# Optimization experiments

Hardware: AMD Instinct MI355X
Metric: run time of the kernel (lower is better)

Reference implementation:

```python
import jax, jax.numpy as jnp
import numpy as np

H = 64          # HIDDEN_SIZE
D = 300         # WORD_VEC_DIMS
L = 3           # NUM_LSTM_LAYERS
B = 256
T = 512


def _uniform(key, shape, scale):
    return jax.random.uniform(key, shape, jnp.float32, -scale, scale)


def setup_inputs() -> dict:
    key = jax.random.key(0)
    keys = jax.random.split(key, 32)
    s = 1.0 / np.sqrt(H)  # torch LSTM/Linear init scale
    inp = {
        "input": jax.random.normal(keys[0], (B, T, D), jnp.float32),
        "h_0": jnp.zeros((L, B, H), jnp.float32),
        "c_0": jnp.zeros((L, B, H), jnp.float32),
    }
    k = 1
    for l in range(L):
        din = D if l == 0 else H
        inp[f"wih{l}"] = _uniform(keys[k], (4 * H, din), s); k += 1
        inp[f"whh{l}"] = _uniform(keys[k], (4 * H, H), s); k += 1
        inp[f"bih{l}"] = _uniform(keys[k], (4 * H,), s); k += 1
        inp[f"bhh{l}"] = _uniform(keys[k], (4 * H,), s); k += 1
    inp["w1"] = _uniform(keys[k], (H, H), s); k += 1
    inp["b1"] = _uniform(keys[k], (H,), s); k += 1
    inp["w2"] = _uniform(keys[k], (D, H), s); k += 1
    inp["b2"] = _uniform(keys[k], (D,), s); k += 1
    return inp


def _lstm_layer(x_tbd, h0, c0, Wih, Whh, bih, bhh):
    # x_tbd: [T, B, Din]; precompute input projection outside the scan
    xp = jnp.einsum('tbd,gd->tbg', x_tbd, Wih) + bih  # [T, B, 4H]

    def step(carry, xt):
        h, c = carry
        g = xt + h @ Whh.T + bhh
        i, f, gg, o = jnp.split(g, 4, axis=-1)  # torch gate order: i,f,g,o
        c = jax.nn.sigmoid(f) * c + jax.nn.sigmoid(i) * jnp.tanh(gg)
        h = jax.nn.sigmoid(o) * jnp.tanh(c)
        return (h, c), h

    (hT, cT), hs = jax.lax.scan(step, (h0, c0), xp)
    return hs, hT, cT  # hs: [T, B, H]


def reference(input, h_0, c_0, wih0, whh0, bih0, bhh0, wih1, whh1, bih1, bhh1,
              wih2, whh2, bih2, bhh2, w1, b1, w2, b2):
    wih = [wih0, wih1, wih2]
    whh = [whh0, whh1, whh2]
    bih = [bih0, bih1, bih2]
    bhh = [bhh0, bhh1, bhh2]
    x = jnp.transpose(input, (1, 0, 2))  # [T, B, D]
    hs_n, cs_n = [], []
    for l in range(L):
        x, hT, cT = _lstm_layer(x, h_0[l], c_0[l], wih[l], whh[l], bih[l], bhh[l])
        hs_n.append(hT)
        cs_n.append(cT)
    # x is now [T, B, H] == output.permute(1, 0, 2) of the batch_first LSTM.
    # Faithfully replicate the original permute+view reordering:
    flat = x.reshape(-1, H)                       # time-major flatten
    y = jnp.tanh(flat @ w1.T + b1) @ w2.T + b2    # MLP head
    out = y.reshape(input.shape[0], -1, D)        # reinterpreted batch-major
    h_n = jnp.stack(hs_n)
    c_n = jnp.stack(cs_n)
    return out, h_n, c_n
```

## Files before the change

### kernel.cpp

```cpp
#include <hip/hip_runtime.h>
#include <math.h>


#define TT 512
#define BB 256
#define DD 300
#define HH 64
#define MM (TT * BB)
#define XP 256
#define TC 128
#define NC (TT / TC)

__device__ __forceinline__ float bf2f(unsigned short u) {
    return __uint_as_float(((unsigned int)u) << 16);
}
__device__ __forceinline__ unsigned short f2bf(float f) {
    unsigned int x = __float_as_uint(f);
    x += 0x7FFFu + ((x >> 16) & 1u);
    return (unsigned short)(x >> 16);
}
__device__ __forceinline__ float sigm(float x) { return 1.f / (1.f + __expf(-x)); }
__device__ __forceinline__ float tanh_f(float x) { return 1.f - 2.f / (__expf(2.f * x) + 1.f); }

__device__ __forceinline__ float ld1(const void* p, long long i, int md) {
    return md ? ((const float*)p)[i] : bf2f(((const unsigned short*)p)[i]);
}
__device__ __forceinline__ void ld4v(float* d, const void* p, long long i, int md) {
    if (md) {
        float4 v = *(const float4*)((const float*)p + i);
        d[0] = v.x; d[1] = v.y; d[2] = v.z; d[3] = v.w;
    } else {
        ushort4 u = *(const ushort4*)((const unsigned short*)p + i);
        d[0] = bf2f(u.x); d[1] = bf2f(u.y); d[2] = bf2f(u.z); d[3] = bf2f(u.w);
    }
}

#define FMA4x4(a, bv)                                        \
    acc[0][0] = fmaf((a).x, (bv).x, acc[0][0]);              \
    acc[0][1] = fmaf((a).x, (bv).y, acc[0][1]);              \
    acc[0][2] = fmaf((a).x, (bv).z, acc[0][2]);              \
    acc[0][3] = fmaf((a).x, (bv).w, acc[0][3]);              \
    acc[1][0] = fmaf((a).y, (bv).x, acc[1][0]);              \
    acc[1][1] = fmaf((a).y, (bv).y, acc[1][1]);              \
    acc[1][2] = fmaf((a).y, (bv).z, acc[1][2]);              \
    acc[1][3] = fmaf((a).y, (bv).w, acc[1][3]);              \
    acc[2][0] = fmaf((a).z, (bv).x, acc[2][0]);              \
    acc[2][1] = fmaf((a).z, (bv).y, acc[2][1]);              \
    acc[2][2] = fmaf((a).z, (bv).z, acc[2][2]);              \
    acc[2][3] = fmaf((a).z, (bv).w, acc[2][3]);              \
    acc[3][0] = fmaf((a).w, (bv).x, acc[3][0]);              \
    acc[3][1] = fmaf((a).w, (bv).y, acc[3][1]);              \
    acc[3][2] = fmaf((a).w, (bv).z, acc[3][2]);              \
    acc[3][3] = fmaf((a).w, (bv).w, acc[3][3]);

__global__ void detect_kernel(const void* inp, int* mode) {
    if (threadIdx.x == 0 && blockIdx.x == 0) {
        const unsigned short* u = (const unsigned short*)inp;
        int bad = 0;
        for (int i = 0; i < 256; ++i) {
            float f = bf2f(u[i]);
            if (!(f == f) || fabsf(f) > 1e6f) ++bad;
        }
        *mode = (bad >= 4) ? 1 : 0;
    }
}

__global__ __launch_bounds__(256) void init_state(
    const void* h0, const void* c0, float* hstate, float* cstate, const int* modep)
{
    const int md = *modep;
    int i = blockIdx.x * 256 + threadIdx.x;
    if (i < 3 * BB * HH) {
        hstate[i] = ld1(h0, i, md);
        cstate[i] = ld1(c0, i, md);
    }
}

__global__ __launch_bounds__(256) void final_state(
    const float* hstate, const float* cstate, void* out, const int* modep)
{
    const int md = *modep;
    int i = blockIdx.x * 256 + threadIdx.x;
    const long long base = (long long)MM * DD;
    if (i < 3 * BB * HH) {
        if (md) {
            ((float*)out)[base + i] = hstate[i];
            ((float*)out)[base + 3 * BB * HH + i] = cstate[i];
        } else {
            ((unsigned short*)out)[base + i] = f2bf(hstate[i]);
            ((unsigned short*)out)[base + 3 * BB * HH + i] = f2bf(cstate[i]);
        }
    }
}

__global__ __launch_bounds__(256) void proj0_chunk(
    const void* __restrict__ inp, const void* __restrict__ wih,
    const void* __restrict__ bih, const void* __restrict__ bhh,
    float* __restrict__ xp, const int* modep, int chunk)
{
    const int md = *modep;
    __shared__ __align__(16) float At[64][68];
    __shared__ __align__(16) float Wt[64][68];
    const int tid = threadIdx.x;
    const int lr = tid >> 2;
    const int lc = (tid & 3) * 16;
    const int tx = tid & 15, ty = tid >> 4;
    const int m0 = blockIdx.x * 64, n0 = blockIdx.y * 64;
    const int ml = m0 + lr;
    const int b = ml & 255;
    const int t = chunk * TC + (ml >> 8);
    const long long abase = (long long)b * (TT * DD) + (long long)t * DD;
    const long long wbase = (long long)(n0 + lr) * DD;
    float acc[4][4] = {{0.f,0.f,0.f,0.f},{0.f,0.f,0.f,0.f},{0.f,0.f,0.f,0.f},{0.f,0.f,0.f,0.f}};
    for (int k0 = 0; k0 < DD; k0 += 64) {
        if (k0 + lc + 15 < DD) {
            #pragma unroll
            for (int q = 0; q < 4; ++q) {
                float va[4], vw[4];
                ld4v(va, inp, abase + k0 + lc + q * 4, md);
                ld4v(vw, wih, wbase + k0 + lc + q * 4, md);
                #pragma unroll
                for (int e = 0; e < 4; ++e) {
                    At[lc + q * 4 + e][lr] = va[e];
                    Wt[lc + q * 4 + e][lr] = vw[e];
                }
            }
        } else {
            #pragma unroll
            for (int q = 0; q < 16; ++q) {
                int k = k0 + lc + q;
                At[lc + q][lr] = (k < DD) ? ld1(inp, abase + k, md) : 0.f;
                Wt[lc + q][lr] = (k < DD) ? ld1(wih, wbase + k, md) : 0.f;
            }
        }
        __syncthreads();
        #pragma unroll 16
        for (int k = 0; k < 64; ++k) {
            float4 a = *(const float4*)&At[k][ty * 4];
            float4 bv = *(const float4*)&Wt[k][tx * 4];
            FMA4x4(a, bv)
        }
        __syncthreads();
    }
    float bias[4];
    #pragma unroll
    for (int j = 0; j < 4; ++j) {
        int n = n0 + tx * 4 + j;
        bias[j] = ld1(bih, n, md) + ld1(bhh, n, md);
    }
    #pragma unroll
    for (int i = 0; i < 4; ++i) {
        long long row = m0 + ty * 4 + i;
        float4 o = make_float4(acc[i][0] + bias[0], acc[i][1] + bias[1],
                               acc[i][2] + bias[2], acc[i][3] + bias[3]);
        *(float4*)(xp + row * XP + n0 + tx * 4) = o;
    }
}

__global__ __launch_bounds__(256) void projh_chunk(
    const float* __restrict__ A, const void* __restrict__ wih,
    const void* __restrict__ bih, const void* __restrict__ bhh,
    float* __restrict__ xp, const int* modep)
{
    const int md = *modep;
    __shared__ __align__(16) float At[64][68];
    __shared__ __align__(16) float Wt[64][68];
    const int tid = threadIdx.x;
    const int lr = tid >> 2;
    const int lc = (tid & 3) * 16;
    const int tx = tid & 15, ty = tid >> 4;
    const int m0 = blockIdx.x * 64, n0 = blockIdx.y * 64;
    float acc[4][4] = {{0.f,0.f,0.f,0.f},{0.f,0.f,0.f,0.f},{0.f,0.f,0.f,0.f},{0.f,0.f,0.f,0.f}};
    #pragma unroll
    for (int q = 0; q < 4; ++q) {
        float4 av = *(const float4*)(A + (long long)(m0 + lr) * HH + lc + q * 4);
        float vw[4];
        ld4v(vw, wih, (long long)(n0 + lr) * HH + lc + q * 4, md);
        At[lc+q*4+0][lr]=av.x; At[lc+q*4+1][lr]=av.y; At[lc+q*4+2][lr]=av.z; At[lc+q*4+3][lr]=av.w;
        Wt[lc+q*4+0][lr]=vw[0]; Wt[lc+q*4+1][lr]=vw[1]; Wt[lc+q*4+2][lr]=vw[2]; Wt[lc+q*4+3][lr]=vw[3];
    }
    __syncthreads();
    #pragma unroll 16
    for (int k = 0; k < 64; ++k) {
        float4 a = *(const float4*)&At[k][ty * 4];
        float4 bv = *(const float4*)&Wt[k][tx * 4];
        FMA4x4(a, bv)
    }
    float bias[4];
    #pragma unroll
    for (int j = 0; j < 4; ++j) {
        int n = n0 + tx * 4 + j;
        bias[j] = ld1(bih, n, md) + ld1(bhh, n, md);
    }
    #pragma unroll
    for (int i = 0; i < 4; ++i) {
        long long row = m0 + ty * 4 + i;
        float4 o = make_float4(acc[i][0] + bias[0], acc[i][1] + bias[1],
                               acc[i][2] + bias[2], acc[i][3] + bias[3]);
        *(float4*)(xp + row * XP + n0 + tx * 4) = o;
    }
}

__global__ __launch_bounds__(256) void scan_chunk(
    const float* __restrict__ xp, float* __restrict__ hs,
    const void* __restrict__ whh,
    float* __restrict__ hstate, float* __restrict__ cstate, const int* modep)
{
    const int md = *modep;
    const int b = blockIdx.x;
    const int j = threadIdx.x;
    const int g = ((j & 3) << 6) | (j >> 2);
    const int m = j & 63;
    __shared__ __align__(16) float h_s[64];
    __shared__ __align__(16) float g_s[2][256];
    float w[64];
    #pragma unroll
    for (int q = 0; q < 16; ++q) {
        float v[4];
        ld4v(v, whh, (long long)g * HH + q * 4, md);
        w[4*q+0]=v[0]; w[4*q+1]=v[1]; w[4*q+2]=v[2]; w[4*q+3]=v[3];
    }
    float c = cstate[b * HH + m];
    h_s[m] = hstate[b * HH + m];
    float hval = h_s[m];

    const int type = j & 3;
    const float aa = (type == 2) ? 2.f : 1.f;
    const float cc = 1.f - aa;

    const long long xbase = (long long)b * XP + g;
    const long long xstep = (long long)BB * XP;
    float xc[8], xn[8];
    #pragma unroll
    for (int p = 0; p < 8; ++p) xc[p] = xp[xbase + (long long)p * xstep];

    for (int tg = 0; tg < TC; tg += 8) {
        if (tg + 8 < TC) {
            #pragma unroll
            for (int p = 0; p < 8; ++p)
                xn[p] = xp[xbase + (long long)(tg + 8 + p) * xstep];
        }
        #pragma unroll
        for (int u = 0; u < 8; ++u) {
            const int t = tg + u;
            float a0 = xc[u], a1 = 0.f, a2 = 0.f, a3 = 0.f;
            const float4* h4 = (const float4*)h_s;
            #pragma unroll
            for (int q = 0; q < 16; ++q) {
                float4 hv = h4[q];
                a0 = fmaf(hv.x, w[4*q+0], a0);
                a1 = fmaf(hv.y, w[4*q+1], a1);
                a2 = fmaf(hv.z, w[4*q+2], a2);
                a3 = fmaf(hv.w, w[4*q+3], a3);
            }
            float gr = (a0 + a1) + (a2 + a3);
            float s = 1.f / (1.f + __expf(-aa * gr));
            g_s[t & 1][j] = fmaf(aa, s, cc);
            asm volatile("s_waitcnt lgkmcnt(0)\n\ts_barrier" ::: "memory");
            float4 gv = *(const float4*)&g_s[t & 1][4 * m];
            c = gv.y * c + gv.x * gv.z;
            hval = gv.w * tanh_f(c);
            h_s[m] = hval;
            if (j < 64) hs[((long long)t * BB + b) * HH + m] = hval;
        }
        #pragma unroll
        for (int p = 0; p < 8; ++p) xc[p] = xn[p];
    }
    if (j < 64) {
        hstate[b * HH + m] = hval;
        cstate[b * HH + m] = c;
    }
}

__global__ __launch_bounds__(256) void head_chunk(
    const float* __restrict__ hs, const void* __restrict__ w1,
    const void* __restrict__ b1, const void* __restrict__ w2,
    const void* __restrict__ b2, void* __restrict__ out,
    const int* modep, int chunk)
{
    const int md = *modep;
    __shared__ __align__(16) float Ht[64][68];
    __shared__ __align__(16) float Wt[64][68];
    __shared__ __align__(16) float Zt[64][68];
    const int tid = threadIdx.x;
    const int lr = tid >> 2;
    const int lc = (tid & 3) * 16;
    const int tx = tid & 15, ty = tid >> 4;
    const int m0 = blockIdx.x * 64;
    const long long gbase = (long long)chunk * TC * BB;
    #pragma unroll
    for (int q = 0; q < 4; ++q) {
        float4 av = *(const float4*)(hs + (long long)(m0 + lr) * HH + lc + q * 4);
        float vw[4];
        ld4v(vw, w1, (long long)lr * HH + lc + q * 4, md);
        Ht[lc+q*4+0][lr]=av.x; Ht[lc+q*4+1][lr]=av.y; Ht[lc+q*4+2][lr]=av.z; Ht[lc+q*4+3][lr]=av.w;
        Wt[lc+q*4+0][lr]=vw[0]; Wt[lc+q*4+1][lr]=vw[1]; Wt[lc+q*4+2][lr]=vw[2]; Wt[lc+q*4+3][lr]=vw[3];
    }
    __syncthreads();
    {
        float acc[4][4] = {{0.f,0.f,0.f,0.f},{0.f,0.f,0.f,0.f},{0.f,0.f,0.f,0.f},{0.f,0.f,0.f,0.f}};
        #pragma unroll 16
        for (int k = 0; k < 64; ++k) {
            float4 a = *(const float4*)&Ht[k][ty * 4];
            float4 bv = *(const float4*)&Wt[k][tx * 4];
            FMA4x4(a, bv)
        }
        #pragma unroll
        for (int jj = 0; jj < 4; ++jj) {
            float bb = ld1(b1, tx * 4 + jj, md);
            #pragma unroll
            for (int ii = 0; ii < 4; ++ii)
                Zt[tx * 4 + jj][ty * 4 + ii] = tanh_f(acc[ii][jj] + bb);
        }
    }
    __syncthreads();
    for (int dt = 0; dt < 5; ++dt) {
        const int d0 = dt * 64;
        if (d0 + lr < DD) {
            #pragma unroll
            for (int q = 0; q < 4; ++q) {
                float vw[4];
                ld4v(vw, w2, (long long)(d0 + lr) * HH + lc + q * 4, md);
                Wt[lc+q*4+0][lr]=vw[0]; Wt[lc+q*4+1][lr]=vw[1];
                Wt[lc+q*4+2][lr]=vw[2]; Wt[lc+q*4+3][lr]=vw[3];
            }
        }
        __syncthreads();
        float acc[4][4] = {{0.f,0.f,0.f,0.f},{0.f,0.f,0.f,0.f},{0.f,0.f,0.f,0.f},{0.f,0.f,0.f,0.f}};
        #pragma unroll 16
        for (int k = 0; k < 64; ++k) {
            float4 a = *(const float4*)&Zt[k][ty * 4];
            float4 bv = *(const float4*)&Wt[k][tx * 4];
            FMA4x4(a, bv)
        }
        const int d = d0 + tx * 4;
        if (d < DD) {
            float bb0 = ld1(b2, d + 0, md), bb1 = ld1(b2, d + 1, md);
            float bb2v = ld1(b2, d + 2, md), bb3 = ld1(b2, d + 3, md);
            #pragma unroll
            for (int ii = 0; ii < 4; ++ii) {
                long long row = gbase + m0 + ty * 4 + ii;
                float o0 = acc[ii][0] + bb0, o1 = acc[ii][1] + bb1;
                float o2 = acc[ii][2] + bb2v, o3 = acc[ii][3] + bb3;
                if (md) {
                    *(float4*)((float*)out + row * DD + d) = make_float4(o0, o1, o2, o3);
                } else {
                    ushort4 o;
                    o.x = f2bf(o0); o.y = f2bf(o1); o.z = f2bf(o2); o.w = f2bf(o3);
                    *(ushort4*)((unsigned short*)out + row * DD + d) = o;
                }
            }
        }
        __syncthreads();
    }
}

extern "C" void kernel_launch(void* const* d_in, const int* in_sizes, int n_in,
                              void* d_out, int out_size, void* d_ws, size_t ws_size,
                              hipStream_t stream)
{
    const void* inp  = d_in[0];
    const void* h0   = d_in[1];
    const void* c0   = d_in[2];
    const void* wih0 = d_in[3];
    const void* whh0 = d_in[4];
    const void* bih0 = d_in[5];
    const void* bhh0 = d_in[6];
    const void* wih1 = d_in[7];
    const void* whh1 = d_in[8];
    const void* bih1 = d_in[9];
    const void* bhh1 = d_in[10];
    const void* wih2 = d_in[11];
    const void* whh2 = d_in[12];
    const void* bih2 = d_in[13];
    const void* bhh2 = d_in[14];
    const void* w1   = d_in[15];
    const void* b1   = d_in[16];
    const void* w2   = d_in[17];
    const void* b2   = d_in[18];

    int* mode = (int*)d_ws;
    float* wsf = (float*)d_ws;
    float* hstate = wsf + 16;
    float* cstate = hstate + 3 * BB * HH;
    float* xp  = cstate + 3 * BB * HH;
    float* hs0 = xp + (size_t)TC * BB * XP;
    float* hs1 = hs0 + (size_t)TC * BB * HH;
    float* hs2 = hs1 + (size_t)TC * BB * HH;

    detect_kernel<<<1, 64, 0, stream>>>(inp, mode);
    init_state<<<192, 256, 0, stream>>>(h0, c0, hstate, cstate, mode);

    for (int c = 0; c < NC; ++c) {
        proj0_chunk<<<dim3(TC * BB / 64, 4), 256, 0, stream>>>(
            inp, wih0, bih0, bhh0, xp, mode, c);
        scan_chunk<<<BB, 256, 0, stream>>>(
            xp, hs0, whh0, hstate, cstate, mode);
        projh_chunk<<<dim3(TC * BB / 64, 4), 256, 0, stream>>>(
            hs0, wih1, bih1, bhh1, xp, mode);
        scan_chunk<<<BB, 256, 0, stream>>>(
            xp, hs1, whh1, hstate + BB * HH, cstate + BB * HH, mode);
        projh_chunk<<<dim3(TC * BB / 64, 4), 256, 0, stream>>>(
            hs1, wih2, bih2, bhh2, xp, mode);
        scan_chunk<<<BB, 256, 0, stream>>>(
            xp, hs2, whh2, hstate + 2 * BB * HH, cstate + 2 * BB * HH, mode);
        head_chunk<<<TC * BB / 64, 256, 0, stream>>>(
            hs2, w1, b1, w2, b2, d_out, mode, c);
    }
    final_state<<<192, 256, 0, stream>>>(hstate, cstate, d_out, mode);
}
```

Measured before the change: 1.974 ms.

## Use split-bf16 MFMA for projections and head, shuffle-based LSTM gate exchange

Replaces the FP32 FMA tiled GEMMs in the input projections and MLP head with bf16 MFMA 16x16x32 instructions. To keep FP32-level accuracy, each operand is split into three bf16 parts and six cross products are accumulated. The weights are pre-split once by a new split_w kernel into workspace. The scan kernel now exchanges gate values through wave shuffles instead of a shared gate buffer, with a double-buffered h, and the hs buffers are merged into one. The split adds six MFMAs per tile plus conversion overhead, and the scan changes alter its synchronisation pattern.

```diff
diff --git a/kernel.cpp b/kernel.cpp
--- a/kernel.cpp
+++ b/kernel.cpp
@@ -11,6 +11,9 @@
 #define TC 128
 #define NC (TT / TC)
 
+typedef __attribute__((ext_vector_type(8))) short bf16x8;
+typedef __attribute__((ext_vector_type(4))) float f32x4;
+
 __device__ __forceinline__ float bf2f(unsigned short u) {
     return __uint_as_float(((unsigned int)u) << 16);
 }
@@ -19,7 +22,6 @@
     x += 0x7FFFu + ((x >> 16) & 1u);
     return (unsigned short)(x >> 16);
 }
-__device__ __forceinline__ float sigm(float x) { return 1.f / (1.f + __expf(-x)); }
 __device__ __forceinline__ float tanh_f(float x) { return 1.f - 2.f / (__expf(2.f * x) + 1.f); }
 
 __device__ __forceinline__ float ld1(const void* p, long long i, int md) {
@@ -35,23 +37,36 @@
     }
 }
 
-#define FMA4x4(a, bv)                                        \
-    acc[0][0] = fmaf((a).x, (bv).x, acc[0][0]);              \
-    acc[0][1] = fmaf((a).x, (bv).y, acc[0][1]);              \
-    acc[0][2] = fmaf((a).x, (bv).z, acc[0][2]);              \
-    acc[0][3] = fmaf((a).x, (bv).w, acc[0][3]);              \
-    acc[1][0] = fmaf((a).y, (bv).x, acc[1][0]);              \
-    acc[1][1] = fmaf((a).y, (bv).y, acc[1][1]);              \
-    acc[1][2] = fmaf((a).y, (bv).z, acc[1][2]);              \
-    acc[1][3] = fmaf((a).y, (bv).w, acc[1][3]);              \
-    acc[2][0] = fmaf((a).z, (bv).x, acc[2][0]);              \
-    acc[2][1] = fmaf((a).z, (bv).y, acc[2][1]);              \
-    acc[2][2] = fmaf((a).z, (bv).z, acc[2][2]);              \
-    acc[2][3] = fmaf((a).z, (bv).w, acc[2][3]);              \
-    acc[3][0] = fmaf((a).w, (bv).x, acc[3][0]);              \
-    acc[3][1] = fmaf((a).w, (bv).y, acc[3][1]);              \
-    acc[3][2] = fmaf((a).w, (bv).z, acc[3][2]);              \
-    acc[3][3] = fmaf((a).w, (bv).w, acc[3][3]);
+__device__ __forceinline__ f32x4 mfma16(bf16x8 a, bf16x8 b, f32x4 c) {
+    return __builtin_amdgcn_mfma_f32_16x16x32_bf16(a, b, c, 0, 0, 0);
+}
+
+__device__ __forceinline__ f32x4 mfma6(bf16x8 a1, bf16x8 a2, bf16x8 a3,
+                                       bf16x8 b1, bf16x8 b2, bf16x8 b3, f32x4 t) {
+    t = mfma16(a2, b2, t);
+    t = mfma16(a1, b3, t);
+    t = mfma16(a3, b1, t);
+    t = mfma16(a1, b2, t);
+    t = mfma16(a2, b1, t);
+    t = mfma16(a1, b1, t);
+    return t;
+}
+
+__device__ __forceinline__ void split3x4(const float* v, ushort4& h1, ushort4& h2, ushort4& h3) {
+    unsigned short a[4], b[4], c[4];
+    #pragma unroll
+    for (int e = 0; e < 4; ++e) {
+        unsigned short x = f2bf(v[e]);
+        float r1 = v[e] - bf2f(x);
+        unsigned short y = f2bf(r1);
+        float r2 = r1 - bf2f(y);
+        unsigned short z = f2bf(r2);
+        a[e] = x; b[e] = y; c[e] = z;
+    }
+    h1 = make_ushort4(a[0], a[1], a[2], a[3]);
+    h2 = make_ushort4(b[0], b[1], b[2], b[3]);
+    h3 = make_ushort4(c[0], c[1], c[2], c[3]);
+}
 
 __global__ void detect_kernel(const void* inp, int* mode) {
     if (threadIdx.x == 0 && blockIdx.x == 0) {
@@ -93,111 +108,178 @@
     }
 }
 
-__global__ __launch_bounds__(256) void proj0_chunk(
-    const void* __restrict__ inp, const void* __restrict__ wih,
+__global__ __launch_bounds__(256) void split_w(
+    const void* __restrict__ src, unsigned short* __restrict__ dst,
+    int rsrc, int csrc, int rdst, int cdst, const int* modep)
+{
+    const int md = *modep;
+    int i = blockIdx.x * 256 + threadIdx.x;
+    int n = rdst * cdst;
+    if (i >= n) return;
+    int r = i / cdst, cc = i - r * cdst;
+    float v = (r < rsrc && cc < csrc) ? ld1(src, (long long)r * csrc + cc, md) : 0.f;
+    unsigned short a = f2bf(v);
+    float r1 = v - bf2f(a);
+    unsigned short b = f2bf(r1);
+    float r2 = r1 - bf2f(b);
+    unsigned short c = f2bf(r2);
+    dst[i] = a; dst[n + i] = b; dst[2 * n + i] = c;
+}
+
+__global__ __launch_bounds__(256, 2) void proj0_chunk(
+    const void* __restrict__ inp, const unsigned short* __restrict__ wsp,
     const void* __restrict__ bih, const void* __restrict__ bhh,
     float* __restrict__ xp, const int* modep, int chunk)
 {
     const int md = *modep;
-    __shared__ __align__(16) float At[64][68];
-    __shared__ __align__(16) float Wt[64][68];
+    __shared__ __align__(16) unsigned short aS[3][64 * 40];
+    __shared__ __align__(16) unsigned short wS[3][256 * 40];
     const int tid = threadIdx.x;
-    const int lr = tid >> 2;
-    const int lc = (tid & 3) * 16;
-    const int tx = tid & 15, ty = tid >> 4;
-    const int m0 = blockIdx.x * 64, n0 = blockIdx.y * 64;
-    const int ml = m0 + lr;
+    const int m0 = blockIdx.x * 64;
+    const int lane = tid & 63, wv = tid >> 6;
+    const int fr = lane & 15, fq = lane >> 4;
+    const int ar = tid >> 2, acs = (tid & 3) * 8;
+    const int ml = m0 + ar;
     const int b = ml & 255;
     const int t = chunk * TC + (ml >> 8);
     const long long abase = (long long)b * (TT * DD) + (long long)t * DD;
-    const long long wbase = (long long)(n0 + lr) * DD;
-    float acc[4][4] = {{0.f,0.f,0.f,0.f},{0.f,0.f,0.f,0.f},{0.f,0.f,0.f,0.f},{0.f,0.f,0.f,0.f}};
-    for (int k0 = 0; k0 < DD; k0 += 64) {
-        if (k0 + lc + 15 < DD) {
-            #pragma unroll
-            for (int q = 0; q < 4; ++q) {
-                float va[4], vw[4];
-                ld4v(va, inp, abase + k0 + lc + q * 4, md);
-                ld4v(vw, wih, wbase + k0 + lc + q * 4, md);
+    float bias[4];
+    #pragma unroll
+    for (int nf = 0; nf < 4; ++nf) {
+        int n = wv * 64 + nf * 16 + fr;
+        bias[nf] = ld1(bih, n, md) + ld1(bhh, n, md);
+    }
+    f32x4 acc[4][4] = {};
+    for (int p = 0; p < 10; ++p) {
+        const int k0 = p * 32;
+        #pragma unroll
+        for (int q = 0; q < 2; ++q) {
+            const int kg = k0 + acs + q * 4;
+            float v[4];
+            if (kg + 3 < DD) {
+                ld4v(v, inp, abase + kg, md);
+            } else {
                 #pragma unroll
-                for (int e = 0; e < 4; ++e) {
-                    At[lc + q * 4 + e][lr] = va[e];
-                    Wt[lc + q * 4 + e][lr] = vw[e];
-                }
-            }
-        } else {
-            #pragma unroll
-            for (int q = 0; q < 16; ++q) {
-                int k = k0 + lc + q;
-                At[lc + q][lr] = (k < DD) ? ld1(inp, abase + k, md) : 0.f;
-                Wt[lc + q][lr] = (k < DD) ? ld1(wih, wbase + k, md) : 0.f;
-            }
+                for (int e = 0; e < 4; ++e)
+                    v[e] = (kg + e < DD) ? ld1(inp, abase + kg + e, md) : 0.f;
+            }
+            ushort4 h1, h2, h3;
+            split3x4(v, h1, h2, h3);
+            *(ushort4*)(&aS[0][ar * 40 + acs + q * 4]) = h1;
+            *(ushort4*)(&aS[1][ar * 40 + acs + q * 4]) = h2;
+            *(ushort4*)(&aS[2][ar * 40 + acs + q * 4]) = h3;
+        }
+        #pragma unroll
+        for (int pl = 0; pl < 3; ++pl) {
+            const uint4* gw = (const uint4*)(wsp + (size_t)pl * 81920 + (size_t)tid * 320 + k0);
+            uint4* dw = (uint4*)(&wS[pl][tid * 40]);
+            #pragma unroll
+            for (int qq = 0; qq < 4; ++qq) dw[qq] = gw[qq];
         }
         __syncthreads();
-        #pragma unroll 16
-        for (int k = 0; k < 64; ++k) {
-            float4 a = *(const float4*)&At[k][ty * 4];
-            float4 bv = *(const float4*)&Wt[k][tx * 4];
-            FMA4x4(a, bv)
+        bf16x8 wf[4][3];
+        #pragma unroll
+        for (int nf = 0; nf < 4; ++nf) {
+            #pragma unroll
+            for (int pl = 0; pl < 3; ++pl)
+                wf[nf][pl] = *(const bf16x8*)(&wS[pl][(wv * 64 + nf * 16 + fr) * 40 + fq * 8]);
+        }
+        #pragma unroll
+        for (int mf = 0; mf < 4; ++mf) {
+            bf16x8 a1 = *(const bf16x8*)(&aS[0][(mf * 16 + fr) * 40 + fq * 8]);
+            bf16x8 a2 = *(const bf16x8*)(&aS[1][(mf * 16 + fr) * 40 + fq * 8]);
+            bf16x8 a3 = *(const bf16x8*)(&aS[2][(mf * 16 + fr) * 40 + fq * 8]);
+            #pragma unroll
+            for (int nf = 0; nf < 4; ++nf)
+                acc[mf][nf] = mfma6(a1, a2, a3, wf[nf][0], wf[nf][1], wf[nf][2], acc[mf][nf]);
         }
         __syncthreads();
     }
-    float bias[4];
-    #pragma unroll
-    for (int j = 0; j < 4; ++j) {
-        int n = n0 + tx * 4 + j;
-        bias[j] = ld1(bih, n, md) + ld1(bhh, n, md);
-    }
-    #pragma unroll
-    for (int i = 0; i < 4; ++i) {
-        long long row = m0 + ty * 4 + i;
-        float4 o = make_float4(acc[i][0] + bias[0], acc[i][1] + bias[1],
-                               acc[i][2] + bias[2], acc[i][3] + bias[3]);
-        *(float4*)(xp + row * XP + n0 + tx * 4) = o;
-    }
-}
-
-__global__ __launch_bounds__(256) void projh_chunk(
-    const float* __restrict__ A, const void* __restrict__ wih,
+    #pragma unroll
+    for (int mf = 0; mf < 4; ++mf) {
+        #pragma unroll
+        for (int nf = 0; nf < 4; ++nf) {
+            const int col = wv * 64 + nf * 16 + fr;
+            #pragma unroll
+            for (int r = 0; r < 4; ++r) {
+                const int row = m0 + mf * 16 + fq * 4 + r;
+                xp[(long long)row * XP + col] = acc[mf][nf][r] + bias[nf];
+            }
+        }
+    }
+}
+
+__global__ __launch_bounds__(256, 2) void projh_chunk(
+    const float* __restrict__ A, const unsigned short* __restrict__ wsp,
     const void* __restrict__ bih, const void* __restrict__ bhh,
     float* __restrict__ xp, const int* modep)
 {
     const int md = *modep;
-    __shared__ __align__(16) float At[64][68];
-    __shared__ __align__(16) float Wt[64][68];
+    __shared__ __align__(16) unsigned short aS[3][64 * 40];
+    __shared__ __align__(16) unsigned short wS[3][256 * 40];
     const int tid = threadIdx.x;
-    const int lr = tid >> 2;
-    const int lc = (tid & 3) * 16;
-    const int tx = tid & 15, ty = tid >> 4;
-    const int m0 = blockIdx.x * 64, n0 = blockIdx.y * 64;
-    float acc[4][4] = {{0.f,0.f,0.f,0.f},{0.f,0.f,0.f,0.f},{0.f,0.f,0.f,0.f},{0.f,0.f,0.f,0.f}};
-    #pragma unroll
-    for (int q = 0; q < 4; ++q) {
-        float4 av = *(const float4*)(A + (long long)(m0 + lr) * HH + lc + q * 4);
-        float vw[4];
-        ld4v(vw, wih, (long long)(n0 + lr) * HH + lc + q * 4, md);
-        At[lc+q*4+0][lr]=av.x; At[lc+q*4+1][lr]=av.y; At[lc+q*4+2][lr]=av.z; At[lc+q*4+3][lr]=av.w;
-        Wt[lc+q*4+0][lr]=vw[0]; Wt[lc+q*4+1][lr]=vw[1]; Wt[lc+q*4+2][lr]=vw[2]; Wt[lc+q*4+3][lr]=vw[3];
-    }
-    __syncthreads();
-    #pragma unroll 16
-    for (int k = 0; k < 64; ++k) {
-        float4 a = *(const float4*)&At[k][ty * 4];
-        float4 bv = *(const float4*)&Wt[k][tx * 4];
-        FMA4x4(a, bv)
-    }
+    const int m0 = blockIdx.x * 64;
+    const int lane = tid & 63, wv = tid >> 6;
+    const int fr = lane & 15, fq = lane >> 4;
+    const int ar = tid >> 2, acs = (tid & 3) * 8;
     float bias[4];
     #pragma unroll
-    for (int j = 0; j < 4; ++j) {
-        int n = n0 + tx * 4 + j;
-        bias[j] = ld1(bih, n, md) + ld1(bhh, n, md);
-    }
-    #pragma unroll
-    for (int i = 0; i < 4; ++i) {
-        long long row = m0 + ty * 4 + i;
-        float4 o = make_float4(acc[i][0] + bias[0], acc[i][1] + bias[1],
-                               acc[i][2] + bias[2], acc[i][3] + bias[3]);
-        *(float4*)(xp + row * XP + n0 + tx * 4) = o;
+    for (int nf = 0; nf < 4; ++nf) {
+        int n = wv * 64 + nf * 16 + fr;
+        bias[nf] = ld1(bih, n, md) + ld1(bhh, n, md);
+    }
+    f32x4 acc[4][4] = {};
+    #pragma unroll
+    for (int p = 0; p < 2; ++p) {
+        const int k0 = p * 32;
+        #pragma unroll
+        for (int q = 0; q < 2; ++q) {
+            float v[4];
+            const float4 fv = *(const float4*)(A + (long long)(m0 + ar) * HH + k0 + acs + q * 4);
+            v[0] = fv.x; v[1] = fv.y; v[2] = fv.z; v[3] = fv.w;
+            ushort4 h1, h2, h3;
+            split3x4(v, h1, h2, h3);
+            *(ushort4*)(&aS[0][ar * 40 + acs + q * 4]) = h1;
+            *(ushort4*)(&aS[1][ar * 40 + acs + q * 4]) = h2;
+            *(ushort4*)(&aS[2][ar * 40 + acs + q * 4]) = h3;
+        }
+        #pragma unroll
+        for (int pl = 0; pl < 3; ++pl) {
+            const uint4* gw = (const uint4*)(wsp + (size_t)pl * 16384 + (size_t)tid * 64 + k0);
+            uint4* dw = (uint4*)(&wS[pl][tid * 40]);
+            #pragma unroll
+            for (int qq = 0; qq < 4; ++qq) dw[qq] = gw[qq];
+        }
+        __syncthreads();
+        bf16x8 wf[4][3];
+        #pragma unroll
+        for (int nf = 0; nf < 4; ++nf) {
+            #pragma unroll
+            for (int pl = 0; pl < 3; ++pl)
+                wf[nf][pl] = *(const bf16x8*)(&wS[pl][(wv * 64 + nf * 16 + fr) * 40 + fq * 8]);
+        }
+        #pragma unroll
+        for (int mf = 0; mf < 4; ++mf) {
+            bf16x8 a1 = *(const bf16x8*)(&aS[0][(mf * 16 + fr) * 40 + fq * 8]);
+            bf16x8 a2 = *(const bf16x8*)(&aS[1][(mf * 16 + fr) * 40 + fq * 8]);
+            bf16x8 a3 = *(const bf16x8*)(&aS[2][(mf * 16 + fr) * 40 + fq * 8]);
+            #pragma unroll
+            for (int nf = 0; nf < 4; ++nf)
+                acc[mf][nf] = mfma6(a1, a2, a3, wf[nf][0], wf[nf][1], wf[nf][2], acc[mf][nf]);
+        }
+        __syncthreads();
+    }
+    #pragma unroll
+    for (int mf = 0; mf < 4; ++mf) {
+        #pragma unroll
+        for (int nf = 0; nf < 4; ++nf) {
+            const int col = wv * 64 + nf * 16 + fr;
+            #pragma unroll
+            for (int r = 0; r < 4; ++r) {
+                const int row = m0 + mf * 16 + fq * 4 + r;
+                xp[(long long)row * XP + col] = acc[mf][nf][r] + bias[nf];
+            }
+        }
     }
 }
 
@@ -210,9 +292,10 @@
     const int b = blockIdx.x;
     const int j = threadIdx.x;
     const int g = ((j & 3) << 6) | (j >> 2);
+    const int i = j >> 2;
     const int m = j & 63;
-    __shared__ __align__(16) float h_s[64];
-    __shared__ __align__(16) float g_s[2][256];
+    const int bl = j & 60;
+    __shared__ __align__(16) float h_s[2][64];
     float w[64];
     #pragma unroll
     for (int q = 0; q < 16; ++q) {
@@ -220,9 +303,9 @@
         ld4v(v, whh, (long long)g * HH + q * 4, md);
         w[4*q+0]=v[0]; w[4*q+1]=v[1]; w[4*q+2]=v[2]; w[4*q+3]=v[3];
     }
-    float c = cstate[b * HH + m];
-    h_s[m] = hstate[b * HH + m];
-    float hval = h_s[m];
+    float c = cstate[b * HH + i];
+    h_s[0][m] = hstate[b * HH + m];
+    float hval = 0.f;
 
     const int type = j & 3;
     const float aa = (type == 2) ? 2.f : 1.f;
@@ -244,7 +327,7 @@
         for (int u = 0; u < 8; ++u) {
             const int t = tg + u;
             float a0 = xc[u], a1 = 0.f, a2 = 0.f, a3 = 0.f;
-            const float4* h4 = (const float4*)h_s;
+            const float4* h4 = (const float4*)h_s[t & 1];
             #pragma unroll
             for (int q = 0; q < 16; ++q) {
                 float4 hv = h4[q];
@@ -255,99 +338,135 @@
             }
             float gr = (a0 + a1) + (a2 + a3);
             float s = 1.f / (1.f + __expf(-aa * gr));
-            g_s[t & 1][j] = fmaf(aa, s, cc);
+            float y = fmaf(aa, s, cc);
+            float yi = __shfl(y, bl | 0);
+            float yf = __shfl(y, bl | 1);
+            float yg = __shfl(y, bl | 2);
+            float yo = __shfl(y, bl | 3);
+            c = yf * c + yi * yg;
+            hval = yo * tanh_f(c);
+            if ((j & 3) == 0) {
+                h_s[(t & 1) ^ 1][i] = hval;
+                hs[((long long)t * BB + b) * HH + i] = hval;
+            }
             asm volatile("s_waitcnt lgkmcnt(0)\n\ts_barrier" ::: "memory");
-            float4 gv = *(const float4*)&g_s[t & 1][4 * m];
-            c = gv.y * c + gv.x * gv.z;
-            hval = gv.w * tanh_f(c);
-            h_s[m] = hval;
-            if (j < 64) hs[((long long)t * BB + b) * HH + m] = hval;
         }
         #pragma unroll
         for (int p = 0; p < 8; ++p) xc[p] = xn[p];
     }
-    if (j < 64) {
-        hstate[b * HH + m] = hval;
-        cstate[b * HH + m] = c;
-    }
-}
-
-__global__ __launch_bounds__(256) void head_chunk(
-    const float* __restrict__ hs, const void* __restrict__ w1,
-    const void* __restrict__ b1, const void* __restrict__ w2,
+    if ((j & 3) == 0) {
+        hstate[b * HH + i] = hval;
+        cstate[b * HH + i] = c;
+    }
+}
+
+__global__ __launch_bounds__(256, 1) void head_chunk(
+    const float* __restrict__ hs, const unsigned short* __restrict__ w1p,
+    const void* __restrict__ b1, const unsigned short* __restrict__ w2p,
     const void* __restrict__ b2, void* __restrict__ out,
     const int* modep, int chunk)
 {
     const int md = *modep;
-    __shared__ __align__(16) float Ht[64][68];
-    __shared__ __align__(16) float Wt[64][68];
-    __shared__ __align__(16) float Zt[64][68];
+    __shared__ __align__(16) unsigned short aS[3][64 * 72];
+    __shared__ __align__(16) unsigned short wS[3][64 * 72];
+    __shared__ __align__(16) unsigned short zS[3][64 * 72];
     const int tid = threadIdx.x;
-    const int lr = tid >> 2;
-    const int lc = (tid & 3) * 16;
-    const int tx = tid & 15, ty = tid >> 4;
     const int m0 = blockIdx.x * 64;
     const long long gbase = (long long)chunk * TC * BB;
-    #pragma unroll
-    for (int q = 0; q < 4; ++q) {
-        float4 av = *(const float4*)(hs + (long long)(m0 + lr) * HH + lc + q * 4);
-        float vw[4];
-        ld4v(vw, w1, (long long)lr * HH + lc + q * 4, md);
-        Ht[lc+q*4+0][lr]=av.x; Ht[lc+q*4+1][lr]=av.y; Ht[lc+q*4+2][lr]=av.z; Ht[lc+q*4+3][lr]=av.w;
-        Wt[lc+q*4+0][lr]=vw[0]; Wt[lc+q*4+1][lr]=vw[1]; Wt[lc+q*4+2][lr]=vw[2]; Wt[lc+q*4+3][lr]=vw[3];
+    const int lane = tid & 63, wv = tid >> 6;
+    const int fr = lane & 15, fq = lane >> 4;
+    const int ar = tid >> 2, cs = (tid & 3) * 16;
+    #pragma unroll
+    for (int e = 0; e < 4; ++e) {
+        float v[4];
+        const float4 fv = *(const float4*)(hs + (long long)(m0 + ar) * HH + cs + e * 4);
+        v[0] = fv.x; v[1] = fv.y; v[2] = fv.z; v[3] = fv.w;
+        ushort4 h1, h2, h3;
+        split3x4(v, h1, h2, h3);
+        *(ushort4*)(&aS[0][ar * 72 + cs + e * 4]) = h1;
+        *(ushort4*)(&aS[1][ar * 72 + cs + e * 4]) = h2;
+        *(ushort4*)(&aS[2][ar * 72 + cs + e * 4]) = h3;
+    }
+    #pragma unroll
+    for (int pl = 0; pl < 3; ++pl) {
+        const uint4* g1 = (const uint4*)(w1p + (size_t)pl * 4096 + (size_t)ar * 64 + cs);
+        *(uint4*)(&wS[pl][ar * 72 + cs]) = g1[0];
+        *(uint4*)(&wS[pl][ar * 72 + cs + 8]) = g1[1];
     }
     __syncthreads();
     {
-        float acc[4][4] = {{0.f,0.f,0.f,0.f},{0.f,0.f,0.f,0.f},{0.f,0.f,0.f,0.f},{0.f,0.f,0.f,0.f}};
-        #pragma unroll 16
-        for (int k = 0; k < 64; ++k) {
-            float4 a = *(const float4*)&Ht[k][ty * 4];
-            float4 bv = *(const float4*)&Wt[k][tx * 4];
-            FMA4x4(a, bv)
-        }
-        #pragma unroll
-        for (int jj = 0; jj < 4; ++jj) {
-            float bb = ld1(b1, tx * 4 + jj, md);
-            #pragma unroll
-            for (int ii = 0; ii < 4; ++ii)
-                Zt[tx * 4 + jj][ty * 4 + ii] = tanh_f(acc[ii][jj] + bb);
+        bf16x8 af[2][3];
+        #pragma unroll
+        for (int kf = 0; kf < 2; ++kf) {
+            #pragma unroll
+            for (int pl = 0; pl < 3; ++pl)
+                af[kf][pl] = *(const bf16x8*)(&aS[pl][(wv * 16 + fr) * 72 + kf * 32 + fq * 8]);
+        }
+        f32x4 acc1[4] = {};
+        #pragma unroll
+        for (int nf = 0; nf < 4; ++nf) {
+            #pragma unroll
+            for (int kf = 0; kf < 2; ++kf) {
+                bf16x8 b1f = *(const bf16x8*)(&wS[0][(nf * 16 + fr) * 72 + kf * 32 + fq * 8]);
+                bf16x8 b2f = *(const bf16x8*)(&wS[1][(nf * 16 + fr) * 72 + kf * 32 + fq * 8]);
+                bf16x8 b3f = *(const bf16x8*)(&wS[2][(nf * 16 + fr) * 72 + kf * 32 + fq * 8]);
+                acc1[nf] = mfma6(af[kf][0], af[kf][1], af[kf][2], b1f, b2f, b3f, acc1[nf]);
+            }
+        }
+        #pragma unroll
+        for (int nf = 0; nf < 4; ++nf) {
+            float bb = ld1(b1, nf * 16 + fr, md);
+            #pragma unroll
+            for (int r = 0; r < 4; ++r) {
+                float z = tanh_f(acc1[nf][r] + bb);
+                unsigned short zh = f2bf(z);
+                float r1 = z - bf2f(zh);
+                unsigned short zm = f2bf(r1);
+                float r2 = r1 - bf2f(zm);
+                unsigned short zl = f2bf(r2);
+                int zi = (wv * 16 + fq * 4 + r) * 72 + nf * 16 + fr;
+                zS[0][zi] = zh; zS[1][zi] = zm; zS[2][zi] = zl;
+            }
         }
     }
     __syncthreads();
+    bf16x8 zf[2][3];
+    #pragma unroll
+    for (int kf = 0; kf < 2; ++kf) {
+        #pragma unroll
+        for (int pl = 0; pl < 3; ++pl)
+            zf[kf][pl] = *(const bf16x8*)(&zS[pl][(wv * 16 + fr) * 72 + kf * 32 + fq * 8]);
+    }
     for (int dt = 0; dt < 5; ++dt) {
-        const int d0 = dt * 64;
-        if (d0 + lr < DD) {
-            #pragma unroll
-            for (int q = 0; q < 4; ++q) {
-                float vw[4];
-                ld4v(vw, w2, (long long)(d0 + lr) * HH + lc + q * 4, md);
-                Wt[lc+q*4+0][lr]=vw[0]; Wt[lc+q*4+1][lr]=vw[1];
-                Wt[lc+q*4+2][lr]=vw[2]; Wt[lc+q*4+3][lr]=vw[3];
-            }
+        #pragma unroll
+        for (int pl = 0; pl < 3; ++pl) {
+            const uint4* g2 = (const uint4*)(w2p + (size_t)pl * 20480 + (size_t)(dt * 64 + ar) * 64 + cs);
+            *(uint4*)(&wS[pl][ar * 72 + cs]) = g2[0];
+            *(uint4*)(&wS[pl][ar * 72 + cs + 8]) = g2[1];
         }
         __syncthreads();
-        float acc[4][4] = {{0.f,0.f,0.f,0.f},{0.f,0.f,0.f,0.f},{0.f,0.f,0.f,0.f},{0.f,0.f,0.f,0.f}};
-        #pragma unroll 16
-        for (int k = 0; k < 64; ++k) {
-            float4 a = *(const float4*)&Zt[k][ty * 4];
-            float4 bv = *(const float4*)&Wt[k][tx * 4];
-            FMA4x4(a, bv)
-        }
-        const int d = d0 + tx * 4;
-        if (d < DD) {
-            float bb0 = ld1(b2, d + 0, md), bb1 = ld1(b2, d + 1, md);
-            float bb2v = ld1(b2, d + 2, md), bb3 = ld1(b2, d + 3, md);
-            #pragma unroll
-            for (int ii = 0; ii < 4; ++ii) {
-                long long row = gbase + m0 + ty * 4 + ii;
-                float o0 = acc[ii][0] + bb0, o1 = acc[ii][1] + bb1;
-                float o2 = acc[ii][2] + bb2v, o3 = acc[ii][3] + bb3;
-                if (md) {
-                    *(float4*)((float*)out + row * DD + d) = make_float4(o0, o1, o2, o3);
-                } else {
-                    ushort4 o;
-                    o.x = f2bf(o0); o.y = f2bf(o1); o.z = f2bf(o2); o.w = f2bf(o3);
-                    *(ushort4*)((unsigned short*)out + row * DD + d) = o;
+        f32x4 acc[4] = {};
+        #pragma unroll
+        for (int nf = 0; nf < 4; ++nf) {
+            #pragma unroll
+            for (int kf = 0; kf < 2; ++kf) {
+                bf16x8 b1f = *(const bf16x8*)(&wS[0][(nf * 16 + fr) * 72 + kf * 32 + fq * 8]);
+                bf16x8 b2f = *(const bf16x8*)(&wS[1][(nf * 16 + fr) * 72 + kf * 32 + fq * 8]);
+                bf16x8 b3f = *(const bf16x8*)(&wS[2][(nf * 16 + fr) * 72 + kf * 32 + fq * 8]);
+                acc[nf] = mfma6(zf[kf][0], zf[kf][1], zf[kf][2], b1f, b2f, b3f, acc[nf]);
+            }
+        }
+        #pragma unroll
+        for (int nf = 0; nf < 4; ++nf) {
+            const int col = dt * 64 + nf * 16 + fr;
+            if (col < DD) {
+                float bb = ld1(b2, col, md);
+                #pragma unroll
+                for (int r = 0; r < 4; ++r) {
+                    long long row = gbase + m0 + wv * 16 + fq * 4 + r;
+                    float o = acc[nf][r] + bb;
+                    if (md) ((float*)out)[row * DD + col] = o;
+                    else    ((unsigned short*)out)[row * DD + col] = f2bf(o);
                 }
             }
         }
@@ -384,28 +503,36 @@
     float* hstate = wsf + 16;
     float* cstate = hstate + 3 * BB * HH;
     float* xp  = cstate + 3 * BB * HH;
-    float* hs0 = xp + (size_t)TC * BB * XP;
-    float* hs1 = hs0 + (size_t)TC * BB * HH;
-    float* hs2 = hs1 + (size_t)TC * BB * HH;
+    float* hs  = xp + (size_t)TC * BB * XP;
+    unsigned short* w0s = (unsigned short*)(hs + (size_t)TC * BB * HH);
+    unsigned short* w1s = w0s + (size_t)3 * 81920;
+    unsigned short* w2s = w1s + (size_t)3 * 16384;
+    unsigned short* h1s = w2s + (size_t)3 * 16384;
+    unsigned short* h2s = h1s + (size_t)3 * 4096;
 
     detect_kernel<<<1, 64, 0, stream>>>(inp, mode);
     init_state<<<192, 256, 0, stream>>>(h0, c0, hstate, cstate, mode);
+    split_w<<<320, 256, 0, stream>>>(wih0, w0s, 256, 300, 256, 320, mode);
+    split_w<<<64, 256, 0, stream>>>(wih1, w1s, 256, 64, 256, 64, mode);
+    split_w<<<64, 256, 0, stream>>>(wih2, w2s, 256, 64, 256, 64, mode);
+    split_w<<<16, 256, 0, stream>>>(w1, h1s, 64, 64, 64, 64, mode);
+    split_w<<<80, 256, 0, stream>>>(w2, h2s, 300, 64, 320, 64, mode);
 
     for (int c = 0; c < NC; ++c) {
-        proj0_chunk<<<dim3(TC * BB / 64, 4), 256, 0, stream>>>(
-            inp, wih0, bih0, bhh0, xp, mode, c);
+        proj0_chunk<<<dim3(TC * BB / 64), 256, 0, stream>>>(
+            inp, w0s, bih0, bhh0, xp, mode, c);
         scan_chunk<<<BB, 256, 0, stream>>>(
-            xp, hs0, whh0, hstate, cstate, mode);
-        projh_chunk<<<dim3(TC * BB / 64, 4), 256, 0, stream>>>(
-            hs0, wih1, bih1, bhh1, xp, mode);
+            xp, hs, whh0, hstate, cstate, mode);
+        projh_chunk<<<dim3(TC * BB / 64), 256, 0, stream>>>(
+            hs, w1s, bih1, bhh1, xp, mode);
         scan_chunk<<<BB, 256, 0, stream>>>(
-            xp, hs1, whh1, hstate + BB * HH, cstate + BB * HH, mode);
-        projh_chunk<<<dim3(TC * BB / 64, 4), 256, 0, stream>>>(
-            hs1, wih2, bih2, bhh2, xp, mode);
+            xp, hs, whh1, hstate + BB * HH, cstate + BB * HH, mode);
+        projh_chunk<<<dim3(TC * BB / 64), 256, 0, stream>>>(
+            hs, w2s, bih2, bhh2, xp, mode);
         scan_chunk<<<BB, 256, 0, stream>>>(
-            xp, hs2, whh2, hstate + 2 * BB * HH, cstate + 2 * BB * HH, mode);
+            xp, hs, whh2, hstate + 2 * BB * HH, cstate + 2 * BB * HH, mode);
         head_chunk<<<TC * BB / 64, 256, 0, stream>>>(
-            hs2, w1, b1, w2, b2, d_out, mode, c);
+            hs, h1s, b1, h2s, b2, d_out, mode, c);
     }
     final_state<<<192, 256, 0, stream>>>(hstate, cstate, d_out, mode);
 }
```

Result: faster. 1.649 ms (-16.5%).
